# Kernel tuning notes

Hardware: AMD Instinct MI355X
Metric: run time of the kernel (lower is better)

Reference implementation:

```python
import jax, jax.numpy as jnp
import numpy as np

N = 50000
C_IN = 64
C_OUT = 64
K = 16
EPS = 1e-5


def _bn(x, g, b, m, v):
    # eval-mode BatchNorm1d over last dim
    return (x - m) * jax.lax.rsqrt(v + EPS) * g + b


def setup_inputs() -> dict:
    key = jax.random.key(0)
    ks = jax.random.split(key, 24)
    def lin(i, fan_in, fan_out):
        s = 1.0 / np.sqrt(fan_in)
        W = jax.random.uniform(ks[i], (fan_in, fan_out), jnp.float32, -s, s)
        b = jax.random.uniform(ks[i + 1], (fan_out,), jnp.float32, -s, s)
        return W, b
    Wq, bq = lin(0, C_IN, C_OUT)
    Wk, bk = lin(2, C_IN, C_OUT)
    Wv, bv = lin(4, C_IN, C_OUT)
    Wp, b_p = lin(6, 3, C_OUT)
    Wg1, bg1 = lin(8, C_OUT, C_OUT)
    Wg2, bg2 = lin(10, C_OUT, C_OUT)
    Wo, bo = lin(12, C_OUT, C_OUT)
    def bn_params(i):
        g = jax.random.uniform(ks[i], (C_OUT,), jnp.float32, 0.5, 1.5)
        b = jax.random.normal(ks[i + 1], (C_OUT,), jnp.float32) * 0.1
        m = jax.random.normal(ks[i + 2], (C_OUT,), jnp.float32) * 0.1
        v = jax.random.uniform(ks[i + 3], (C_OUT,), jnp.float32, 0.5, 1.5)
        return g, b, m, v
    bnp_g, bnp_b, bnp_m, bnp_v = bn_params(14)
    bng_g, bng_b, bng_m, bng_v = bn_params(18)
    points = jax.random.normal(ks[22], (N, 3), jnp.float32)
    features = jax.random.normal(ks[23], (N, C_IN), jnp.float32)
    grouped_indices = jax.random.randint(jax.random.fold_in(key, 7), (N, K), 0, N, jnp.int64 if jax.config.jax_enable_x64 else jnp.int32)
    return dict(points=points, features=features, grouped_indices=grouped_indices,
                Wq=Wq, bq=bq, Wk=Wk, bk=bk, Wv=Wv, bv=bv, Wp=Wp, b_p=b_p,
                bnp_g=bnp_g, bnp_b=bnp_b, bnp_m=bnp_m, bnp_v=bnp_v,
                Wg1=Wg1, bg1=bg1, bng_g=bng_g, bng_b=bng_b, bng_m=bng_m, bng_v=bng_v,
                Wg2=Wg2, bg2=bg2, Wo=Wo, bo=bo)


def reference(points, features, grouped_indices,
              Wq, bq, Wk, bk, Wv, bv, Wp, b_p,
              bnp_g, bnp_b, bnp_m, bnp_v,
              Wg1, bg1, bng_g, bng_b, bng_m, bng_v,
              Wg2, bg2, Wo, bo):
    q = features @ Wq + bq                      # (N, C)
    k = features @ Wk + bk
    v = features @ Wv + bv
    gpts = points[grouped_indices]              # (N, K, 3) gather
    gk = k[grouped_indices]                     # (N, K, C)
    gv = v[grouped_indices]                     # (N, K, C)
    rel = gpts - points[:, None, :]             # (N, K, 3)
    p = jax.nn.relu(_bn(rel @ Wp + b_p, bnp_g, bnp_b, bnp_m, bnp_v))  # (N, K, C)
    a = q[:, None, :] - gk + p                  # (N, K, C)
    h = jax.nn.relu(_bn(a @ Wg1 + bg1, bng_g, bng_b, bng_m, bng_v)) @ Wg2 + bg2
    attn = jax.nn.softmax(h, axis=1)            # softmax over neighbor axis
    out = jnp.sum((gv + p) * attn, axis=1) @ Wo + bo  # (N, C)
    return out
```

## Files before the change

kernel.cpp:

```cpp
#include <hip/hip_runtime.h>
#include <hip/hip_bf16.h>

#define EPSV 1e-5f
#define TW 4
#define TPW 8
#define SPD 76

typedef __attribute__((ext_vector_type(8))) short s8v;
typedef __attribute__((ext_vector_type(4))) float f4v;

struct InP {
  const float *points, *features; const int* gidx;
  const float *Wq,*bq,*Wk,*bk,*Wv,*bv,*Wp,*b_p;
  const float *bnp_g,*bnp_b,*bnp_m,*bnp_v;
  const float *Wg1,*bg1,*bng_g,*bng_b,*bng_m,*bng_v;
  const float *Wg2,*bg2,*Wo,*bo;
  float* out; int N;
};
struct WS {
  unsigned short *qW1;
  unsigned short *kvT;
  unsigned short *WAf, *Wkf, *Wvf, *W1f, *W2f, *Wof;
  unsigned short *Wpf;
  float *bq1F, *bpF;
};

__device__ __forceinline__ unsigned short f2bf(float x){
  __hip_bfloat16 h = __float2bfloat16(x);
  unsigned short u; __builtin_memcpy(&u, &h, 2); return u;
}
__device__ __forceinline__ float bf2f(unsigned short s){
  union{unsigned u; float f;} c; c.u = ((unsigned)s) << 16; return c.f;
}
__device__ __forceinline__ unsigned pk2(float x, float y){
  __hip_bfloat162 h = __float22bfloat162_rn(make_float2(x, y));
  unsigned u; __builtin_memcpy(&u, &h, 4); return u;
}
__device__ __forceinline__ s8v pack8(f4v x0, f4v x1){
  s8v r;
  ((unsigned*)&r)[0] = pk2(x0[0], x0[1]);
  ((unsigned*)&r)[1] = pk2(x0[2], x0[3]);
  ((unsigned*)&r)[2] = pk2(x1[0], x1[1]);
  ((unsigned*)&r)[3] = pk2(x1[2], x1[3]);
  return r;
}
__device__ __forceinline__ s8v sub8bf(s8v p, s8v k){
  s8v r;
  #pragma unroll
  for (int t = 0; t < 4; t++){
    float a0 = bf2f((unsigned short)p[2*t+0]) - bf2f((unsigned short)k[2*t+0]);
    float a1 = bf2f((unsigned short)p[2*t+1]) - bf2f((unsigned short)k[2*t+1]);
    ((unsigned*)&r)[t] = pk2(a0, a1);
  }
  return r;
}

__global__ void __launch_bounds__(256) prep_kernel(InP P, WS W){
  const int g = blockIdx.x*256 + threadIdx.x;
  const int e = g >> 3, j = g & 7;
  const int f = e >> 6, L = e & 63;
  const int ks = f & 1, nt = f >> 1;
  const int n = nt*16 + (L & 15);
  const int k = ks*32 + ((L >> 4) << 3) + j;
  const float sg = P.bng_g[n] * rsqrtf(P.bng_v[n] + EPSV);
  W.W1f[e*8+j] = f2bf(P.Wg1[k*64+n] * sg);
  W.W2f[e*8+j] = f2bf(P.Wg2[k*64+n]);
  W.Wof[e*8+j] = f2bf(P.Wo [k*64+n]);
  W.Wkf[e*8+j] = f2bf(P.Wk [k*64+n]);
  W.Wvf[e*8+j] = f2bf(P.Wv [k*64+n]);
  float acc = 0.f;
  #pragma unroll 8
  for (int d = 0; d < 64; d++) acc += P.Wq[k*64+d] * P.Wg1[d*64+n];
  W.WAf[e*8+j] = f2bf(acc * sg);
  if (g < 2048){
    int ep = g >> 3;
    int ntp = ep >> 6, Lp = ep & 63;
    int np_ = ntp*16 + (Lp & 15);
    int kp = ((Lp >> 4) << 3) + j;
    float sp = P.bnp_g[np_] * rsqrtf(P.bnp_v[np_] + EPSV);
    W.Wpf[ep*8+j] = f2bf(kp < 3 ? P.Wp[kp*64+np_]*sp : 0.f);
  }
  if (g < 64){
    float sgt = P.bng_g[g] * rsqrtf(P.bng_v[g] + EPSV);
    float spt = P.bnp_g[g] * rsqrtf(P.bnp_v[g] + EPSV);
    float acc2 = 0.f;
    for (int d = 0; d < 64; d++) acc2 += P.bq[d] * P.Wg1[d*64+g];
    W.bq1F[g] = acc2*sgt + P.bg1[g]*sgt + P.bng_b[g] - P.bng_m[g]*sgt;
    W.bpF[g]  = P.b_p[g]*spt + P.bnp_b[g] - P.bnp_m[g]*spt;
  }
}

__global__ void __launch_bounds__(256) qkv_kernel(InP P, WS W){
  const int tid = threadIdx.x;
  const int wid = tid >> 6, l = tid & 63;
  const int cl = l & 15, q = l >> 4;
  const int TILES = (P.N + 15) >> 4;
  const int task = blockIdx.x * TW + wid;
  if (task >= TILES) return;
  const int i0 = task * 16;
  int row = i0 + cl; if (row > P.N - 1) row = P.N - 1;
  const float* fr = P.features + (size_t)row*64 + q*8;
  f4v x0 = *(const f4v*)fr;
  f4v x1 = *(const f4v*)(fr + 4);
  s8v fa0 = pack8(x0, x1);
  x0 = *(const f4v*)(fr + 32);
  x1 = *(const f4v*)(fr + 36);
  s8v fa1 = pack8(x0, x1);

  auto doMat = [&](const unsigned short* Bf_, const float* biasPtr,
                   unsigned short* outPtr, int stride){
    const s8v* Bf = (const s8v*)Bf_;
    #pragma unroll
    for (int nt = 0; nt < 4; nt++){
      float bn = biasPtr[nt*16 + cl];
      f4v ci = { bn, bn, bn, bn };
      f4v c = __builtin_amdgcn_mfma_f32_16x16x32_bf16(fa0, Bf[(2*nt+0)*64 + l], ci, 0, 0, 0);
      c = __builtin_amdgcn_mfma_f32_16x16x32_bf16(fa1, Bf[(2*nt+1)*64 + l], c, 0, 0, 0);
      #pragma unroll
      for (int r = 0; r < 4; r++){
        int rg = i0 + q*4 + r;
        if (rg < P.N) outPtr[(size_t)rg*stride + nt*16 + cl] = f2bf(c[r]);
      }
    }
  };
  doMat(W.WAf, W.bq1F, W.qW1,      64);
  doMat(W.Wkf, P.bk,   W.kvT,     128);
  doMat(W.Wvf, P.bv,   W.kvT + 64,128);
}

__global__ void __launch_bounds__(256, 2) main_kernel(InP P, WS W){
  __shared__ __align__(16) unsigned short Sp[TW][16*SPD];
  __shared__ __align__(16) unsigned short PreB[TW][TPW*SPD];
  __shared__ __align__(16) int sI[TW][TPW*16];
  const int tid = threadIdx.x;
  const int wid = tid >> 6, l = tid & 63;
  const int cl = l & 15, q = l >> 4;
  const int TILES = (P.N + TPW - 1) / TPW;
  const int task = blockIdx.x * TW + wid;
  if (task >= TILES) return;
  const int i0 = task * TPW;
  unsigned short* Spw = Sp[wid];
  unsigned short* PreBw = PreB[wid];
  int* sIw = sI[wid];

  {
    long base = (long)i0*16 + l*2;
    long maxb = (long)P.N*16 - 2;
    if (base > maxb) base = maxb;
    int2 gi = *(const int2*)(P.gidx + base);
    *(int2*)&sIw[l*2] = gi;
  }

  s8v w1f[8], w2f[8], wpf[4];
  {
    const s8v* W1p = (const s8v*)W.W1f;
    const s8v* W2p = (const s8v*)W.W2f;
    const s8v* Wpp = (const s8v*)W.Wpf;
    #pragma unroll
    for (int f = 0; f < 8; f++){ w1f[f] = W1p[f*64 + l]; w2f[f] = W2p[f*64 + l]; }
    #pragma unroll
    for (int f = 0; f < 4; f++) wpf[f] = Wpp[f*64 + l];
  }
  float bp4[4], b24[4];
  #pragma unroll
  for (int nt = 0; nt < 4; nt++){ bp4[nt] = W.bpF[nt*16 + cl]; b24[nt] = P.bg2[nt*16 + cl]; }

  int nidx = sIw[cl];
  s8v ngk0, ngk1;
  {
    const s8v* kv = (const s8v*)(W.kvT + (size_t)nidx*128);
    ngk0 = kv[q]; ngk1 = kv[4+q];
  }
  float ngx=0.f, ngy=0.f, ngz=0.f;
  if (l < 16){ const float* gp = P.points + (size_t)nidx*3; ngx=gp[0]; ngy=gp[1]; ngz=gp[2]; }
  float ncx = P.points[(size_t)i0*3+0];
  float ncy = P.points[(size_t)i0*3+1];
  float ncz = P.points[(size_t)i0*3+2];
  float nq0, nq1, nq2, nq3;
  {
    const unsigned short* qr = W.qW1 + (size_t)i0*64;
    nq0 = bf2f(qr[cl]); nq1 = bf2f(qr[16+cl]); nq2 = bf2f(qr[32+cl]); nq3 = bf2f(qr[48+cl]);
  }

  #pragma unroll 1
  for (int pt = 0; pt < TPW; pt++){
    s8v gk0=ngk0, gk1=ngk1;
    float gx=ngx, gy=ngy, gz=ngz, cx=ncx, cy=ncy, cz=ncz;
    float qc0=nq0, qc1=nq1, qc2=nq2, qc3=nq3;
    const int iCur = i0 + pt;
    const bool valid = (iCur < P.N);

    unsigned short vv[16];
    {
      int4 vidx = *(const int4*)&sIw[pt*16 + q*4];
      #pragma unroll
      for (int r = 0; r < 4; r++){
        const unsigned short* vb = W.kvT + (size_t)vidx[r]*128 + 64 + cl;
        #pragma unroll
        for (int nt = 0; nt < 4; nt++) vv[nt*4+r] = vb[nt*16];
      }
    }

    s8v ap;
    ((unsigned*)&ap)[0] = pk2(gx-cx, gy-cy);
    ((unsigned*)&ap)[1] = pk2(gz-cz, 0.f);
    ((unsigned*)&ap)[2] = 0u; ((unsigned*)&ap)[3] = 0u;
    f4v pc[4];
    #pragma unroll
    for (int nt = 0; nt < 4; nt++){
      f4v ci = { bp4[nt], bp4[nt], bp4[nt], bp4[nt] };
      pc[nt] = __builtin_amdgcn_mfma_f32_16x16x32_bf16(ap, wpf[nt], ci, 0, 0, 0);
    }
    unsigned pcp[8];
    #pragma unroll
    for (int nt = 0; nt < 4; nt++){
      #pragma unroll
      for (int r = 0; r < 4; r++){
        pc[nt][r] = fmaxf(pc[nt][r], 0.f);
        Spw[(q*4+r)*SPD + nt*16 + cl] = f2bf(pc[nt][r]);
      }
      pcp[nt*2+0] = pk2(pc[nt][0], pc[nt][1]);
      pcp[nt*2+1] = pk2(pc[nt][2], pc[nt][3]);
    }

    {
      int np = (pt + 1) & (TPW-1);
      nidx = sIw[np*16 + cl];
      const s8v* kv = (const s8v*)(W.kvT + (size_t)nidx*128);
      ngk0 = kv[q]; ngk1 = kv[4+q];
      if (l < 16){ const float* gp = P.points + (size_t)nidx*3; ngx=gp[0]; ngy=gp[1]; ngz=gp[2]; }
      int ii = i0 + np; if (ii > P.N - 1) ii = P.N - 1;
      ncx = P.points[(size_t)ii*3+0];
      ncy = P.points[(size_t)ii*3+1];
      ncz = P.points[(size_t)ii*3+2];
      const unsigned short* qr = W.qW1 + (size_t)ii*64;
      nq0 = bf2f(qr[cl]); nq1 = bf2f(qr[16+cl]); nq2 = bf2f(qr[32+cl]); nq3 = bf2f(qr[48+cl]);
    }

    s8v af0, af1;
    {
      s8v p0 = *(const s8v*)&Spw[cl*SPD + q*8];
      s8v p1 = *(const s8v*)&Spw[cl*SPD + 32 + q*8];
      af0 = sub8bf(p0, gk0);
      af1 = sub8bf(p1, gk1);
    }

    f4v tc[4];
    #pragma unroll
    for (int nt = 0; nt < 4; nt++){
      float qcn = (nt==0) ? qc0 : (nt==1) ? qc1 : (nt==2) ? qc2 : qc3;
      f4v ci = { qcn, qcn, qcn, qcn };
      tc[nt] = __builtin_amdgcn_mfma_f32_16x16x32_bf16(af0, w1f[2*nt+0], ci, 0, 0, 0);
      tc[nt] = __builtin_amdgcn_mfma_f32_16x16x32_bf16(af1, w1f[2*nt+1], tc[nt], 0, 0, 0);
      #pragma unroll
      for (int r = 0; r < 4; r++) tc[nt][r] = fmaxf(tc[nt][r], 0.f);
    }

    #pragma unroll
    for (int nt = 0; nt < 4; nt++)
      #pragma unroll
      for (int r = 0; r < 4; r++)
        Spw[(q*4+r)*SPD + nt*16 + cl] = f2bf(tc[nt][r]);
    s8v tf0 = *(const s8v*)&Spw[cl*SPD + q*8];
    s8v tf1 = *(const s8v*)&Spw[cl*SPD + 32 + q*8];

    f4v hc[4];
    #pragma unroll
    for (int nt = 0; nt < 4; nt++){
      f4v ci = { b24[nt], b24[nt], b24[nt], b24[nt] };
      hc[nt] = __builtin_amdgcn_mfma_f32_16x16x32_bf16(tf0, w2f[2*nt+0], ci, 0, 0, 0);
      hc[nt] = __builtin_amdgcn_mfma_f32_16x16x32_bf16(tf1, w2f[2*nt+1], hc[nt], 0, 0, 0);
    }

    float pre4[4];
    #pragma unroll
    for (int nt = 0; nt < 4; nt++){
      float p01lo = bf2f((unsigned short)(pcp[nt*2+0] & 0xffff));
      float p01hi = bf2f((unsigned short)(pcp[nt*2+0] >> 16));
      float p23lo = bf2f((unsigned short)(pcp[nt*2+1] & 0xffff));
      float p23hi = bf2f((unsigned short)(pcp[nt*2+1] >> 16));
      float pv[4] = { p01lo, p01hi, p23lo, p23hi };
      float s = 0.f, acc = 0.f;
      #pragma unroll
      for (int r = 0; r < 4; r++){
        float e2 = __expf(hc[nt][r]);
        s += e2;
        acc = fmaf(e2, bf2f(vv[nt*4+r]) + pv[r], acc);
      }
      s += __shfl_xor(s, 16, 64);
      s += __shfl_xor(s, 32, 64);
      acc += __shfl_xor(acc, 16, 64);
      acc += __shfl_xor(acc, 32, 64);
      pre4[nt] = acc * __builtin_amdgcn_rcpf(s);
    }
    if (valid){
      float sa = (l & 16) ? pre4[1] : pre4[0];
      float sb = (l & 16) ? pre4[3] : pre4[2];
      PreBw[pt*SPD + l] = f2bf((l & 32) ? sb : sa);
    }
  }

  s8v wof[8];
  {
    const s8v* Wop = (const s8v*)W.Wof;
    #pragma unroll
    for (int f = 0; f < 8; f++) wof[f] = Wop[f*64 + l];
  }
  s8v ef0 = *(const s8v*)&PreBw[(cl & 7)*SPD + q*8];
  s8v ef1 = *(const s8v*)&PreBw[(cl & 7)*SPD + 32 + q*8];
  #pragma unroll
  for (int nt = 0; nt < 4; nt++){
    float bn = P.bo[nt*16 + cl];
    f4v ci = { bn, bn, bn, bn };
    f4v oc = __builtin_amdgcn_mfma_f32_16x16x32_bf16(ef0, wof[2*nt+0], ci, 0, 0, 0);
    oc = __builtin_amdgcn_mfma_f32_16x16x32_bf16(ef1, wof[2*nt+1], oc, 0, 0, 0);
    #pragma unroll
    for (int r = 0; r < 4; r++){
      int ro = q*4 + r;
      int rg = i0 + ro;
      if (ro < TPW && rg < P.N) P.out[(size_t)rg*64 + nt*16 + cl] = oc[r];
    }
  }
}

extern "C" void kernel_launch(void* const* d_in, const int* in_sizes, int n_in,
                              void* d_out, int out_size, void* d_ws, size_t ws_size,
                              hipStream_t stream){
  InP P;
  P.points   = (const float*)d_in[0];
  P.features = (const float*)d_in[1];
  P.gidx     = (const int*)d_in[2];
  P.Wq  = (const float*)d_in[3];  P.bq  = (const float*)d_in[4];
  P.Wk  = (const float*)d_in[5];  P.bk  = (const float*)d_in[6];
  P.Wv  = (const float*)d_in[7];  P.bv  = (const float*)d_in[8];
  P.Wp  = (const float*)d_in[9];  P.b_p = (const float*)d_in[10];
  P.bnp_g = (const float*)d_in[11]; P.bnp_b = (const float*)d_in[12];
  P.bnp_m = (const float*)d_in[13]; P.bnp_v = (const float*)d_in[14];
  P.Wg1 = (const float*)d_in[15]; P.bg1 = (const float*)d_in[16];
  P.bng_g = (const float*)d_in[17]; P.bng_b = (const float*)d_in[18];
  P.bng_m = (const float*)d_in[19]; P.bng_v = (const float*)d_in[20];
  P.Wg2 = (const float*)d_in[21]; P.bg2 = (const float*)d_in[22];
  P.Wo  = (const float*)d_in[23]; P.bo  = (const float*)d_in[24];
  P.out = (float*)d_out;
  const int N = in_sizes[0] / 3;
  P.N = N;

  WS W;
  char* w = (char*)d_ws;
  W.qW1 = (unsigned short*)w; w += (size_t)N*64*2;
  W.kvT = (unsigned short*)w; w += (size_t)N*128*2;
  W.WAf = (unsigned short*)w; w += 8*64*8*2;
  W.Wkf = (unsigned short*)w; w += 8*64*8*2;
  W.Wvf = (unsigned short*)w; w += 8*64*8*2;
  W.W1f = (unsigned short*)w; w += 8*64*8*2;
  W.W2f = (unsigned short*)w; w += 8*64*8*2;
  W.Wof = (unsigned short*)w; w += 8*64*8*2;
  W.Wpf = (unsigned short*)w; w += 4*64*8*2;
  W.bq1F = (float*)w; w += 256;
  W.bpF  = (float*)w; w += 256;

  const int TILES16 = (N + 15) / 16;
  const int grid16 = (TILES16 + TW - 1) / TW;
  const int TILES8 = (N + TPW - 1) / TPW;
  const int grid8 = (TILES8 + TW - 1) / TW;
  hipLaunchKernelGGL(prep_kernel, dim3(16),     dim3(256), 0, stream, P, W);
  hipLaunchKernelGGL(qkv_kernel,  dim3(grid16), dim3(256), 0, stream, P, W);
  hipLaunchKernelGGL(main_kernel, dim3(grid8),  dim3(256), 0, stream, P, W);
}
```

Baseline: 206.2 us.

## Halve points per wave, raise occupancy, and double-buffer the LDS scratch

Cuts points per wave task from 8 to 4, which doubles the grid, and raises launch bounds from 2 to 5 blocks per CU. The k-row gather no longer runs one iteration ahead; it is issued at the top of each iteration, and the point loop is unrolled by 2. The positional scratch in shared memory is double-buffered by iteration parity so unrolled iterations do not clash. The aim is more waves in flight to hide gather latency, at the cost of fewer registers per thread (spill risk) and more repeated weight-fragment loads per point.

```diff
diff --git a/kernel.cpp b/kernel.cpp
--- a/kernel.cpp
+++ b/kernel.cpp
@@ -3,7 +3,7 @@
 
 #define EPSV 1e-5f
 #define TW 4
-#define TPW 8
+#define TPW 4
 #define SPD 76
 
 typedef __attribute__((ext_vector_type(8))) short s8v;
@@ -128,8 +128,8 @@
   doMat(W.Wvf, P.bv,   W.kvT + 64,128);
 }
 
-__global__ void __launch_bounds__(256, 2) main_kernel(InP P, WS W){
-  __shared__ __align__(16) unsigned short Sp[TW][16*SPD];
+__global__ void __launch_bounds__(256, 5) main_kernel(InP P, WS W){
+  __shared__ __align__(16) unsigned short Sp[TW][2][16*SPD];
   __shared__ __align__(16) unsigned short PreB[TW][TPW*SPD];
   __shared__ __align__(16) int sI[TW][TPW*16];
   const int tid = threadIdx.x;
@@ -139,16 +139,14 @@
   const int task = blockIdx.x * TW + wid;
   if (task >= TILES) return;
   const int i0 = task * TPW;
-  unsigned short* Spw = Sp[wid];
   unsigned short* PreBw = PreB[wid];
   int* sIw = sI[wid];
 
   {
-    long base = (long)i0*16 + l*2;
-    long maxb = (long)P.N*16 - 2;
+    long base = (long)i0*16 + l;
+    long maxb = (long)P.N*16 - 1;
     if (base > maxb) base = maxb;
-    int2 gi = *(const int2*)(P.gidx + base);
-    *(int2*)&sIw[l*2] = gi;
+    sIw[l] = P.gidx[base];
   }
 
   s8v w1f[8], w2f[8], wpf[4];
@@ -165,14 +163,11 @@
   #pragma unroll
   for (int nt = 0; nt < 4; nt++){ bp4[nt] = W.bpF[nt*16 + cl]; b24[nt] = P.bg2[nt*16 + cl]; }
 
-  int nidx = sIw[cl];
-  s8v ngk0, ngk1;
-  {
-    const s8v* kv = (const s8v*)(W.kvT + (size_t)nidx*128);
-    ngk0 = kv[q]; ngk1 = kv[4+q];
-  }
   float ngx=0.f, ngy=0.f, ngz=0.f;
-  if (l < 16){ const float* gp = P.points + (size_t)nidx*3; ngx=gp[0]; ngy=gp[1]; ngz=gp[2]; }
+  {
+    int nidx = sIw[cl];
+    if (l < 16){ const float* gp = P.points + (size_t)nidx*3; ngx=gp[0]; ngy=gp[1]; ngz=gp[2]; }
+  }
   float ncx = P.points[(size_t)i0*3+0];
   float ncy = P.points[(size_t)i0*3+1];
   float ncz = P.points[(size_t)i0*3+2];
@@ -182,13 +177,13 @@
     nq0 = bf2f(qr[cl]); nq1 = bf2f(qr[16+cl]); nq2 = bf2f(qr[32+cl]); nq3 = bf2f(qr[48+cl]);
   }
 
-  #pragma unroll 1
+  #pragma unroll 2
   for (int pt = 0; pt < TPW; pt++){
-    s8v gk0=ngk0, gk1=ngk1;
-    float gx=ngx, gy=ngy, gz=ngz, cx=ncx, cy=ncy, cz=ncz;
-    float qc0=nq0, qc1=nq1, qc2=nq2, qc3=nq3;
-    const int iCur = i0 + pt;
-    const bool valid = (iCur < P.N);
+    unsigned short* Spw = Sp[wid][pt & 1];
+
+    int kidx = sIw[pt*16 + cl];
+    const s8v* kvp = (const s8v*)(W.kvT + (size_t)kidx*128);
+    s8v gk0 = kvp[q], gk1 = kvp[4+q];
 
     unsigned short vv[16];
     {
@@ -200,6 +195,10 @@
         for (int nt = 0; nt < 4; nt++) vv[nt*4+r] = vb[nt*16];
       }
     }
+
+    float gx=ngx, gy=ngy, gz=ngz, cx=ncx, cy=ncy, cz=ncz;
+    float qc0=nq0, qc1=nq1, qc2=nq2, qc3=nq3;
+    const bool valid = (i0 + pt < P.N);
 
     s8v ap;
     ((unsigned*)&ap)[0] = pk2(gx-cx, gy-cy);
@@ -225,9 +224,7 @@
 
     {
       int np = (pt + 1) & (TPW-1);
-      nidx = sIw[np*16 + cl];
-      const s8v* kv = (const s8v*)(W.kvT + (size_t)nidx*128);
-      ngk0 = kv[q]; ngk1 = kv[4+q];
+      int nidx = sIw[np*16 + cl];
       if (l < 16){ const float* gp = P.points + (size_t)nidx*3; ngx=gp[0]; ngy=gp[1]; ngz=gp[2]; }
       int ii = i0 + np; if (ii > P.N - 1) ii = P.N - 1;
       ncx = P.points[(size_t)ii*3+0];
@@ -306,8 +303,8 @@
     #pragma unroll
     for (int f = 0; f < 8; f++) wof[f] = Wop[f*64 + l];
   }
-  s8v ef0 = *(const s8v*)&PreBw[(cl & 7)*SPD + q*8];
-  s8v ef1 = *(const s8v*)&PreBw[(cl & 7)*SPD + 32 + q*8];
+  s8v ef0 = *(const s8v*)&PreBw[(cl & (TPW-1))*SPD + q*8];
+  s8v ef1 = *(const s8v*)&PreBw[(cl & (TPW-1))*SPD + 32 + q*8];
   #pragma unroll
   for (int nt = 0; nt < 4; nt++){
     float bn = P.bo[nt*16 + cl];
@@ -361,9 +358,9 @@
 
   const int TILES16 = (N + 15) / 16;
   const int grid16 = (TILES16 + TW - 1) / TW;
-  const int TILES8 = (N + TPW - 1) / TPW;
-  const int grid8 = (TILES8 + TW - 1) / TW;
+  const int TILESM = (N + TPW - 1) / TPW;
+  const int gridM = (TILESM + TW - 1) / TW;
   hipLaunchKernelGGL(prep_kernel, dim3(16),     dim3(256), 0, stream, P, W);
   hipLaunchKernelGGL(qkv_kernel,  dim3(grid16), dim3(256), 0, stream, P, W);
-  hipLaunchKernelGGL(main_kernel, dim3(grid8),  dim3(256), 0, stream, P, W);
-}
+  hipLaunchKernelGGL(main_kernel, dim3(gridM),  dim3(256), 0, stream, P, W);
+}
```

Result: slower. 428.2 us (+107.7%).
